# Kernel optimization log

Measured on AMD Instinct MI355X. Metric: run time of the kernel, lower is better.

Reference implementation:

```python
import jax, jax.numpy as jnp
import numpy as np

B, N, E, D = 2, 8192, 1024, 128   # batch, seq, embed_dim, expand_ratio (= head dim)
H = E // D                        # 8 heads (f_proj output dim)
CHUNK = 64
LN_EPS = 1e-5


def _gla_chunked(q, k, v, log_f):
    """Chunked simple GLA: S_t = exp(log_f_t) * S_{t-1} + k_t v_t^T ; o_t = q_t @ S_t.
    q,k,v: [b,h,n,d], log_f: [b,h,n] (log of per-head scalar decay in (0,1))."""
    b, h, n, d = q.shape
    nc = n // CHUNK
    qc = q.reshape(b, h, nc, CHUNK, d)
    kc = k.reshape(b, h, nc, CHUNK, d)
    vc = v.reshape(b, h, nc, CHUNK, d)
    gf = log_f.reshape(b, h, nc, CHUNK)
    g = jnp.cumsum(gf, axis=-1)          # inclusive within-chunk cum log decay [b,h,nc,C]
    gl = g[..., -1]                      # total chunk log decay [b,h,nc]

    # intra-chunk: A[i,j] = (q_i . k_j) * exp(g_i - g_j), j <= i  (g decreasing -> stable)
    mask = jnp.tril(jnp.ones((CHUNK, CHUNK), bool))
    A = jnp.einsum('bhcid,bhcjd->bhcij', qc, kc)
    A = jnp.where(mask, A * jnp.exp(g[..., :, None] - g[..., None, :]), 0.0)
    o_intra = jnp.einsum('bhcij,bhcjd->bhcid', A, vc)

    # inter-chunk: scan over chunks carrying state S [b,h,d,d]
    def step(S, inp):
        q_c, k_c, v_c, g_c, gl_c = inp   # [b,h,C,d],[b,h,C,d],[b,h,C,d],[b,h,C],[b,h]
        o = jnp.einsum('bhid,bhde->bhie', q_c * jnp.exp(g_c)[..., None], S)
        kd = k_c * jnp.exp(gl_c[..., None] - g_c)[..., None]
        S = jnp.exp(gl_c)[..., None, None] * S + jnp.einsum('bhid,bhie->bhde', kd, v_c)
        return S, o

    xs = (jnp.moveaxis(qc, 2, 0), jnp.moveaxis(kc, 2, 0), jnp.moveaxis(vc, 2, 0),
          jnp.moveaxis(g, 2, 0), jnp.moveaxis(gl, 2, 0))
    S0 = jnp.zeros((b, h, d, d), q.dtype)
    _, o_inter = jax.lax.scan(step, S0, xs)      # [nc,b,h,C,d]
    o_inter = jnp.moveaxis(o_inter, 0, 2)        # [b,h,nc,C,d]
    return (o_intra + o_inter).reshape(b, h, n, d)


def setup_inputs() -> dict:
    key = jax.random.key(0)
    ks = jax.random.split(key, 13)
    s = E ** -0.5
    x = jax.random.normal(ks[0], (B, N, E), jnp.float32)
    # per-head lower bound in (0,1), stored in log space as consumed by the module
    log_lower_bound = jnp.log(jax.random.uniform(ks[1], (H,), jnp.float32, 0.05, 0.95))
    Wq = jax.random.normal(ks[2], (E, E), jnp.float32) * s
    Wk = jax.random.normal(ks[3], (E, E), jnp.float32) * s
    Wv = jax.random.normal(ks[4], (E, E), jnp.float32) * s
    Wf = jax.random.normal(ks[5], (E, H), jnp.float32) * s
    Wb1 = jax.random.normal(ks[6], (E, D), jnp.float32) * s
    Wb2 = jax.random.normal(ks[7], (D, E), jnp.float32) * (D ** -0.5)
    Wg1 = jax.random.normal(ks[8], (E, D), jnp.float32) * s
    Wg2 = jax.random.normal(ks[9], (D, E), jnp.float32) * (D ** -0.5)
    Wo = jax.random.normal(ks[10], (E, E), jnp.float32) * s
    ln_scale = jnp.ones((E,), jnp.float32)
    ln_bias = jnp.zeros((E,), jnp.float32)
    return dict(x=x, log_lower_bound=log_lower_bound, Wq=Wq, Wk=Wk, Wv=Wv, Wf=Wf,
                Wb1=Wb1, Wb2=Wb2, Wg1=Wg1, Wg2=Wg2, Wo=Wo,
                ln_scale=ln_scale, ln_bias=ln_bias)


def reference(x, log_lower_bound, Wq, Wk, Wv, Wf, Wb1, Wb2, Wg1, Wg2, Wo, ln_scale, ln_bias):
    silu = jax.nn.silu
    q = silu(x @ Wq)
    k = silu(x @ Wk)
    v = x @ Wv
    f_pre = x @ Wf                               # [B,N,H] per-head decay logits

    # dense-memory Householder-style reflection of q
    beta = silu((x @ Wb1) @ Wb2)
    nb = jnp.sqrt(jnp.sum(beta * beta, axis=-1, keepdims=True))
    beta = beta / jnp.maximum(nb, 1e-6) / (E ** 0.5)
    q = q - 2.0 * jnp.sum(q * beta, axis=-1, keepdims=True) * beta

    def split(t):
        return t.reshape(B, N, H, D).transpose(0, 2, 1, 3)   # [B,H,N,D]
    qh, kh, vh = split(q), split(k), split(v)

    lb = jnp.exp(log_lower_bound)                            # [H]
    f = lb + (1.0 - lb) * jax.nn.sigmoid(f_pre)              # [B,N,H]
    log_f = jnp.log(f).transpose(0, 2, 1)                    # [B,H,N]

    o = _gla_chunked(qh, kh, vh, log_f)                      # [B,H,N,D]
    o = o.transpose(0, 2, 1, 3).reshape(B, N, E)

    gate = jax.nn.sigmoid((x @ Wg1) @ Wg2)
    o = o * gate

    mu = jnp.mean(o, axis=-1, keepdims=True)
    var = jnp.var(o, axis=-1, keepdims=True)
    o = (o - mu) / jnp.sqrt(var + LN_EPS) * ln_scale + ln_bias
    return o @ Wo
```

## Files before the change

kernel.cpp:

```cpp
#include <hip/hip_runtime.h>
#include <hip/hip_bf16.h>
#include <cstdint>


using u16 = unsigned short;
using u32 = unsigned int;
using u64 = unsigned long long;

typedef __attribute__((ext_vector_type(8))) short s16x8;
typedef __attribute__((ext_vector_type(4))) float f32x4;

__device__ __forceinline__ float b2f(u16 b){ u32 u = ((u32)b)<<16; return __builtin_bit_cast(float,u); }
__device__ __forceinline__ u16 f2b(float f){
  u32 u = __builtin_bit_cast(u32,f);
  return (u16)((u + 0x7FFFu + ((u>>16)&1u)) >> 16);
}
__device__ __forceinline__ float sigm(float x){ return 1.f/(1.f + __expf(-x)); }
__device__ __forceinline__ float silu(float x){ return x * sigm(x); }

__device__ __forceinline__ void gload16(const void* g, void* l){
  __builtin_amdgcn_global_load_lds((const __attribute__((address_space(1))) void*)g,
                                   (__attribute__((address_space(3))) void*)l, 16, 0, 0);
}
#define MFMA(a,b,c) __builtin_amdgcn_mfma_f32_16x16x32_bf16((a),(b),(c),0,0,0)

__device__ __forceinline__ void swz_block(int& bx, int& by){
  const int gx = gridDim.x;
  const int nwg = gx * gridDim.y;
  int lin = by*gx + bx;
  const int cpx = nwg >> 3;
  lin = (lin & 7)*cpx + (lin >> 3);
  bx = lin % gx; by = lin / gx;
}

__global__ __launch_bounds__(256) void fill_diag(float* __restrict__ p, int n, float val){
  int i = blockIdx.x*256 + threadIdx.x;
  if (i < n) p[i] = val;
}

__global__ __launch_bounds__(256) void cast_bf(const float4* __restrict__ src,
                                               ushort4* __restrict__ dst, int n4){
  int i = blockIdx.x*256 + threadIdx.x;
  int st = gridDim.x*256;
  for (; i < n4; i += st){
    float4 v = src[i];
    ushort4 o; o.x=f2b(v.x); o.y=f2b(v.y); o.z=f2b(v.z); o.w=f2b(v.w);
    dst[i] = o;
  }
}

__global__ __launch_bounds__(256) void wprep(const float* __restrict__ src,
                                             u16* __restrict__ dst, int K, int Nsrc){
  __shared__ float t[64][65];
  const int k0 = blockIdx.x*64, n0 = blockIdx.y*64;
  const int tid = threadIdx.x;
  #pragma unroll
  for (int e=0;e<16;e++){
    int idx = e*256 + tid;
    int r = idx>>6, c = idx&63;
    float v = 0.f;
    if (n0 + c < Nsrc) v = src[(u64)(k0+r)*Nsrc + n0 + c];
    t[r][c] = v;
  }
  __syncthreads();
  #pragma unroll
  for (int e=0;e<16;e++){
    int idx = e*256 + tid;
    int nn = idx>>6, kk = idx&63;
    dst[(u64)(n0+nn)*K + k0 + kk] = f2b(t[kk][nn]);
  }
}

__global__ __launch_bounds__(256,4) void gemm_bt(const u16* __restrict__ A, int lda,
                                                 const u16* __restrict__ Bt,
                                                 void* __restrict__ C, int ldc,
                                                 int K, int mode){
  __shared__ __align__(16) u16 As[128*64];
  __shared__ __align__(16) u16 Bs[128*64];
  const int tid = threadIdx.x, lane = tid&63, wid = tid>>6;
  int bx = blockIdx.x, by = blockIdx.y;
  swz_block(bx, by);
  const int bn0 = bx*128, bm0 = by*128;
  const int wr = wid>>1, wc = wid&1;
  const int g = lane>>4, ln = lane&15;

  f32x4 acc[4][4];
  #pragma unroll
  for (int i=0;i<4;i++)
    #pragma unroll
    for (int j=0;j<4;j++) acc[i][j] = f32x4{0.f,0.f,0.f,0.f};

  const int nk = K >> 6;
  for (int kt = 0; kt < nk; ++kt){
    const int k0 = kt<<6;
    #pragma unroll
    for (int j=0;j<4;j++){
      const int p = (wid*4+j)*64 + lane;
      const int row = p>>3, sl = p&7;
      const int sc = ((sl ^ (row&7))<<3);
      gload16(A  + (u64)(bm0+row)*lda + k0 + sc, (char*)As + (wid*4+j)*1024);
      gload16(Bt + (u64)(bn0+row)*K   + k0 + sc, (char*)Bs + (wid*4+j)*1024);
    }
    __syncthreads();
    #pragma unroll
    for (int ks=0;ks<2;ks++){
      s16x8 af[4], bf[4];
      #pragma unroll
      for (int mt=0;mt<4;mt++){
        const int row = wr*64 + mt*16 + ln;
        af[mt] = *(const s16x8*)(As + row*64 + (((ks*4+g) ^ (row&7))<<3));
      }
      #pragma unroll
      for (int nt=0;nt<4;nt++){
        const int row = wc*64 + nt*16 + ln;
        bf[nt] = *(const s16x8*)(Bs + row*64 + (((ks*4+g) ^ (row&7))<<3));
      }
      #pragma unroll
      for (int mt=0;mt<4;mt++)
        #pragma unroll
        for (int nt=0;nt<4;nt++)
          acc[mt][nt] = MFMA(af[mt], bf[nt], acc[mt][nt]);
    }
    __syncthreads();
  }
  if (mode == 0){
    float* Cf = (float*)C;
    #pragma unroll
    for (int mt=0;mt<4;mt++)
      #pragma unroll
      for (int nt=0;nt<4;nt++){
        const int col = bn0 + wc*64 + nt*16 + ln;
        #pragma unroll
        for (int r=0;r<4;r++){
          const u64 row = (u64)(bm0 + wr*64 + mt*16 + g*4 + r);
          Cf[row*ldc + col] = acc[mt][nt][r];
        }
      }
  } else {
    u16* Cb = (u16*)C;
    #pragma unroll
    for (int mt=0;mt<4;mt++)
      #pragma unroll
      for (int nt=0;nt<4;nt++){
        const int col = bn0 + wc*64 + nt*16 + ln;
        #pragma unroll
        for (int r=0;r<4;r++){
          const u64 row = (u64)(bm0 + wr*64 + mt*16 + g*4 + r);
          Cb[row*ldc + col] = f2b(acc[mt][nt][r]);
        }
      }
  }
}

__global__ __launch_bounds__(256,4) void gemm_proj(const u16* __restrict__ A,
                                                   const u16* __restrict__ Bt,
                                                   u16* __restrict__ Qb,
                                                   u16* __restrict__ Kp,
                                                   u16* __restrict__ KT,
                                                   u16* __restrict__ VT,
                                                   u16* __restrict__ FP,
                                                   const float* __restrict__ Gp,
                                                   const float* __restrict__ GLp){
  __shared__ __align__(16) u16 As[128*64];
  __shared__ __align__(16) u16 Bs[128*64];
  const int tid = threadIdx.x, lane = tid&63, wid = tid>>6;
  int bx = blockIdx.x, by = blockIdx.y;
  swz_block(bx, by);
  const int bn0 = bx*128, bm0 = by*128;
  const int wr = wid>>1, wc = wid&1;
  const int g = lane>>4, ln = lane&15;

  f32x4 acc[4][4];
  #pragma unroll
  for (int i=0;i<4;i++)
    #pragma unroll
    for (int j=0;j<4;j++) acc[i][j] = f32x4{0.f,0.f,0.f,0.f};

  for (int kt = 0; kt < 16; ++kt){
    const int k0 = kt<<6;
    #pragma unroll
    for (int j=0;j<4;j++){
      const int p = (wid*4+j)*64 + lane;
      const int row = p>>3, sl = p&7;
      const int sc = ((sl ^ (row&7))<<3);
      gload16(A  + (u64)(bm0+row)*1024 + k0 + sc, (char*)As + (wid*4+j)*1024);
      gload16(Bt + (u64)(bn0+row)*1024 + k0 + sc, (char*)Bs + (wid*4+j)*1024);
    }
    __syncthreads();
    #pragma unroll
    for (int ks=0;ks<2;ks++){
      s16x8 af[4], bf[4];
      #pragma unroll
      for (int mt=0;mt<4;mt++){
        const int row = wr*64 + mt*16 + ln;
        af[mt] = *(const s16x8*)(As + row*64 + (((ks*4+g) ^ (row&7))<<3));
      }
      #pragma unroll
      for (int nt=0;nt<4;nt++){
        const int row = wc*64 + nt*16 + ln;
        bf[nt] = *(const s16x8*)(Bs + row*64 + (((ks*4+g) ^ (row&7))<<3));
      }
      #pragma unroll
      for (int mt=0;mt<4;mt++)
        #pragma unroll
        for (int nt=0;nt<4;nt++)
          acc[mt][nt] = MFMA(af[mt], bf[nt], acc[mt][nt]);
    }
    __syncthreads();
  }

  const int cb = bn0 >> 7;
  if (cb < 8){
    #pragma unroll
    for (int mt=0;mt<4;mt++)
      #pragma unroll
      for (int nt=0;nt<4;nt++){
        const int col = bn0 + wc*64 + nt*16 + ln;
        #pragma unroll
        for (int r=0;r<4;r++)
          Qb[(u64)(bm0 + wr*64 + mt*16 + g*4 + r)*1024 + col] = f2b(acc[mt][nt][r]);
      }
  } else if (cb < 16){
    const int h = cb - 8;
    const int bh = (bm0>>13)*8 + h;
    const int trowb = (bm0 & 8191) + wr*64;
    const float gl = GLp[bh*128 + (trowb>>6)];
    float es[4][4];
    #pragma unroll
    for (int mt=0;mt<4;mt++)
      #pragma unroll
      for (int r=0;r<4;r++)
        es[mt][r] = __expf(gl - Gp[(u64)bh*8192 + trowb + mt*16 + g*4 + r]);
    #pragma unroll
    for (int mt=0;mt<4;mt++){
      const int trow = trowb + mt*16 + g*4;
      #pragma unroll
      for (int nt=0;nt<4;nt++){
        const int d = wc*64 + nt*16 + ln;
        ushort4 o; u16* op = (u16*)&o;
        #pragma unroll
        for (int r=0;r<4;r++){
          const float s = silu(acc[mt][nt][r]);
          op[r] = f2b(s * es[mt][r]);
          Kp[(u64)(bm0 + wr*64 + mt*16 + g*4 + r)*1024 + h*128 + d] = f2b(s);
        }
        *(ushort4*)(KT + ((u64)bh*128 + d)*8192 + trow) = o;
      }
    }
  } else if (cb < 24){
    const int h = cb - 16;
    const int bh = (bm0>>13)*8 + h;
    const int trowb = (bm0 & 8191) + wr*64;
    #pragma unroll
    for (int mt=0;mt<4;mt++){
      const int trow = trowb + mt*16 + g*4;
      #pragma unroll
      for (int nt=0;nt<4;nt++){
        const int d = wc*64 + nt*16 + ln;
        ushort4 o; u16* op = (u16*)&o;
        #pragma unroll
        for (int r=0;r<4;r++) op[r] = f2b(acc[mt][nt][r]);
        *(ushort4*)(VT + ((u64)bh*128 + d)*8192 + trow) = o;
      }
    }
  } else {
    const int off = (cb == 24) ? 0 : 128;
    #pragma unroll
    for (int mt=0;mt<4;mt++)
      #pragma unroll
      for (int nt=0;nt<4;nt++){
        const int col = off + wc*64 + nt*16 + ln;
        #pragma unroll
        for (int r=0;r<4;r++)
          FP[(u64)(bm0 + wr*64 + mt*16 + g*4 + r)*384 + col] = f2b(acc[mt][nt][r]);
      }
  }
}

__global__ __launch_bounds__(64) void fkernel(const u16* __restrict__ FP,
                                              const float* __restrict__ llb,
                                              float* __restrict__ G, float* __restrict__ GL){
  const int c = blockIdx.x, bh = blockIdx.y;
  const int b = bh>>3, h = bh&7;
  const int t = threadIdx.x;
  const int tok = c*64 + t;
  const float fp = b2f(FP[(u64)(b*8192 + tok)*384 + 256 + h]);
  const float lb = __expf(llb[h]);
  const float f = lb + (1.f - lb) * sigm(fp);
  float x = __logf(f);
  #pragma unroll
  for (int d=1; d<64; d<<=1){
    float v = __shfl_up(x, d);
    if (t >= d) x += v;
  }
  G[(u64)bh*8192 + tok] = x;
  const float gl = __shfl(x, 63);
  if (t == 0) GL[bh*128 + c] = gl;
}

__global__ __launch_bounds__(256) void e1_reflect(u16* __restrict__ Q,
                                                  const u16* __restrict__ BP){
  const u64 t = blockIdx.x;
  const int tid = threadIdx.x;
  __shared__ float red[8];
  u16* qrow = Q + t*1024;
  const u16* brow = BP + t*1024;
  ushort4 qv = ((const ushort4*)qrow)[tid];
  ushort4 bv = ((const ushort4*)brow)[tid];
  u16* qp = (u16*)&qv; const u16* bp = (const u16*)&bv;
  float q[4], bb[4];
  float s1 = 0.f, s2 = 0.f;
  #pragma unroll
  for (int j=0;j<4;j++){
    const float qq = silu(b2f(qp[j]));
    const float bbv = silu(b2f(bp[j]));
    q[j] = qq; bb[j] = bbv;
    s1 += bbv*bbv; s2 += qq*bbv;
  }
  #pragma unroll
  for (int d=1; d<64; d<<=1){ s1 += __shfl_xor(s1,d); s2 += __shfl_xor(s2,d); }
  const int wid = tid>>6, lane = tid&63;
  if (lane==0){ red[wid]=s1; red[4+wid]=s2; }
  __syncthreads();
  s1 = red[0]+red[1]+red[2]+red[3];
  s2 = red[4]+red[5]+red[6]+red[7];
  const float bs = 1.f/(fmaxf(sqrtf(s1), 1e-6f) * 32.f);
  const float coef = 2.f * s2 * bs * bs;
  #pragma unroll
  for (int j=0;j<4;j++) qp[j] = f2b(q[j] - coef*bb[j]);
  ((ushort4*)qrow)[tid] = qv;
}

__global__ __launch_bounds__(256,4) void g1_local(const u16* __restrict__ KT,
                                                  const u16* __restrict__ VT,
                                                  u16* __restrict__ LT){
  __shared__ __align__(16) u16 kts[128*64];
  __shared__ __align__(16) u16 vts[128*64];
  const int c = blockIdx.x, bh = blockIdx.y;
  const int tid = threadIdx.x, lane = tid&63, wid = tid>>6;
  const int g = lane>>4, ln = lane&15;
  #pragma unroll
  for (int j=0;j<4;j++){
    const int p = (wid*4+j)*64 + lane;
    const int row = p>>3, sl = p&7;
    const int sc = ((sl ^ (row&7))<<3);
    gload16(KT + ((u64)bh*128 + row)*8192 + (u64)c*64 + sc, (char*)kts + (wid*4+j)*1024);
    gload16(VT + ((u64)bh*128 + row)*8192 + (u64)c*64 + sc, (char*)vts + (wid*4+j)*1024);
  }
  __syncthreads();
  f32x4 acc[2][8];
  #pragma unroll
  for (int mt=0;mt<2;mt++)
    #pragma unroll
    for (int dt=0;dt<8;dt++) acc[mt][dt] = f32x4{0.f,0.f,0.f,0.f};
  #pragma unroll
  for (int kk=0;kk<2;kk++){
    s16x8 av[2];
    #pragma unroll
    for (int mt=0;mt<2;mt++){
      const int row = wid*32 + mt*16 + ln;
      av[mt] = *(const s16x8*)(vts + row*64 + (((kk*4+g) ^ (row&7))<<3));
    }
    #pragma unroll
    for (int dt=0;dt<8;dt++){
      const int row = dt*16 + ln;
      const s16x8 bk = *(const s16x8*)(kts + row*64 + (((kk*4+g) ^ (row&7))<<3));
      #pragma unroll
      for (int mt=0;mt<2;mt++) acc[mt][dt] = MFMA(av[mt], bk, acc[mt][dt]);
    }
  }
  u16* out = LT + ((u64)(bh*128 + c)<<14);
  #pragma unroll
  for (int mt=0;mt<2;mt++)
    #pragma unroll
    for (int dt=0;dt<8;dt++){
      const int d = dt*16 + ln;
      #pragma unroll
      for (int r=0;r<4;r++){
        const int n = wid*32 + mt*16 + g*4 + r;
        out[n*128 + d] = f2b(acc[mt][dt][r]);
      }
    }
}

__global__ __launch_bounds__(256) void g2_scan(u16* __restrict__ LS,
                                               const float* __restrict__ GL){
  __shared__ float egl[128];
  const int bh = blockIdx.y;
  if (threadIdx.x < 128) egl[threadIdx.x] = __expf(GL[bh*128 + threadIdx.x]);
  __syncthreads();
  const u64 e = (u64)blockIdx.x*256 + threadIdx.x;
  u16* P = LS + ((u64)bh<<21) + e;
  float s = 0.f;
  for (int c=0;c<128;c++){
    const float l = b2f(P[(u64)c<<14]);
    P[(u64)c<<14] = f2b(s);
    s = egl[c]*s + l;
  }
}

__global__ __launch_bounds__(256,2) void g3_out(const u16* __restrict__ Qb,
                                                const u16* __restrict__ Kp,
                                                const u16* __restrict__ VT,
                                                const u16* __restrict__ SBb,
                                                const float* __restrict__ Gb,
                                                u16* __restrict__ O){
  __shared__ __align__(16) u16 qs[64*128];
  __shared__ __align__(16) u16 ks[64*128];
  __shared__ __align__(16) u16 vts[128*64];
  __shared__ __align__(16) u16 sbs[64*128];
  __shared__ __align__(16) u16 Ast[4][16*64];
  __shared__ float gg[64];
  const int c = blockIdx.x, bh = blockIdx.y;
  const int b = bh>>3, h = bh&7;
  const int tid = threadIdx.x, lane = tid&63, wid = tid>>6;
  const int g = lane>>4, ln = lane&15;
  const u64 trow0 = (u64)b*8192 + (u64)c*64;

  if (tid < 64) gg[tid] = Gb[(u64)bh*8192 + c*64 + tid];

  const u16* sbbase = SBb + ((u64)(bh*128 + c)<<14);
  #pragma unroll
  for (int j=0;j<4;j++){
    const int p = (wid*4+j)*64 + lane;
    const int row = p>>4, sl = p&15;
    const int sc = ((sl ^ (row&7))<<3);
    gload16(Qb + (trow0 + row)*1024 + h*128 + sc, (char*)qs + (wid*4+j)*1024);
    gload16(Kp + (trow0 + row)*1024 + h*128 + sc, (char*)ks + (wid*4+j)*1024);
    const int row2 = p>>3, sl2 = p&7;
    gload16(VT + ((u64)bh*128 + row2)*8192 + (u64)c*64 + ((sl2 ^ (row2&7))<<3),
            (char*)vts + (wid*4+j)*1024);
    gload16(sbbase + row*128 + sc, (char*)sbs + (wid*4+j)*1024);
  }
  __syncthreads();

  f32x4 pa[4];
  #pragma unroll
  for (int jt=0;jt<4;jt++) pa[jt] = f32x4{0.f,0.f,0.f,0.f};
  #pragma unroll
  for (int kk=0;kk<4;kk++){
    const int arow = wid*16 + ln;
    const s16x8 aq = *(const s16x8*)(qs + arow*128 + (((kk*4+g) ^ (arow&7))<<3));
    #pragma unroll
    for (int jt=0;jt<4;jt++){
      const int brow = jt*16 + ln;
      const s16x8 bk = *(const s16x8*)(ks + brow*128 + (((kk*4+g) ^ (brow&7))<<3));
      pa[jt] = MFMA(aq, bk, pa[jt]);
    }
  }
  #pragma unroll
  for (int jt=0;jt<4;jt++){
    const int jj = jt*16 + ln;
    const float gj = gg[jj];
    #pragma unroll
    for (int r=0;r<4;r++){
      const int il = g*4 + r;
      const int ii = wid*16 + il;
      const float v = (jj <= ii) ? pa[jt][r] * __expf(gg[ii] - gj) : 0.f;
      Ast[wid][il*64 + (((jj>>3) ^ (il&7))<<3) + (jj&7)] = f2b(v);
    }
  }
  {
    const int row = wid*16 + (lane>>2);
    const float sc = __expf(gg[row]);
    u16* base = qs + row*128 + (lane&3)*32;
    #pragma unroll
    for (int ee=0; ee<4; ee++){
      s16x8 v = *(s16x8*)(base + ee*8);
      u16* vp = (u16*)&v;
      #pragma unroll
      for (int xj=0;xj<8;xj++) vp[xj] = f2b(b2f(vp[xj]) * sc);
      *(s16x8*)(base + ee*8) = v;
    }
  }
  f32x4 acc[8];
  #pragma unroll
  for (int i=0;i<8;i++) acc[i] = f32x4{0.f,0.f,0.f,0.f};
  #pragma unroll
  for (int kk=0;kk<2;kk++){
    const s16x8 aa = *(const s16x8*)(Ast[wid] + ln*64 + (((kk*4+g) ^ (ln&7))<<3));
    #pragma unroll
    for (int nt=0;nt<8;nt++){
      const int brow = nt*16 + ln;
      const s16x8 bb = *(const s16x8*)(vts + brow*64 + (((kk*4+g) ^ (brow&7))<<3));
      acc[nt] = MFMA(aa, bb, acc[nt]);
    }
  }
  #pragma unroll
  for (int kk=0;kk<4;kk++){
    const int arow = wid*16 + ln;
    const s16x8 aq = *(const s16x8*)(qs + arow*128 + (((kk*4+g) ^ (arow&7))<<3));
    #pragma unroll
    for (int nt=0;nt<4;nt++){
      const int brow = nt*16 + ln;
      const s16x8 bs = *(const s16x8*)(sbs + brow*128 + (((kk*4+g) ^ (brow&7))<<3));
      acc[nt] = MFMA(aq, bs, acc[nt]);
    }
  }
  __syncthreads();
  #pragma unroll
  for (int j=0;j<4;j++){
    const int p = (wid*4+j)*64 + lane;
    const int row = p>>4, sl = p&15;
    gload16(sbbase + 8192 + row*128 + ((sl ^ (row&7))<<3), (char*)sbs + (wid*4+j)*1024);
  }
  __syncthreads();
  #pragma unroll
  for (int kk=0;kk<4;kk++){
    const int arow = wid*16 + ln;
    const s16x8 aq = *(const s16x8*)(qs + arow*128 + (((kk*4+g) ^ (arow&7))<<3));
    #pragma unroll
    for (int nt=0;nt<4;nt++){
      const int brow = nt*16 + ln;
      const s16x8 bs = *(const s16x8*)(sbs + brow*128 + (((kk*4+g) ^ (brow&7))<<3));
      acc[4+nt] = MFMA(aq, bs, acc[4+nt]);
    }
  }
  u16* outp = O + trow0*1024 + h*128;
  #pragma unroll
  for (int nt=0;nt<8;nt++){
    const int n = nt*16 + ln;
    #pragma unroll
    for (int r=0;r<4;r++){
      const int i = wid*16 + g*4 + r;
      outp[(u64)i*1024 + n] = f2b(acc[nt][r]);
    }
  }
}

__global__ __launch_bounds__(256) void e2_ln(const u16* __restrict__ O,
                                             const u16* __restrict__ GP,
                                             const float* __restrict__ lnsc,
                                             const float* __restrict__ lnbi,
                                             u16* __restrict__ OL){
  const u64 t = blockIdx.x;
  const int tid = threadIdx.x;
  __shared__ float red[8];
  ushort4 ov = ((const ushort4*)(O + t*1024))[tid];
  ushort4 gv = ((const ushort4*)(GP + t*1024))[tid];
  const u16* ovp = (const u16*)&ov;
  const u16* gvp = (const u16*)&gv;
  float o[4]; float s = 0.f, s2 = 0.f;
  #pragma unroll
  for (int j=0;j<4;j++){
    const float val = b2f(ovp[j]) * sigm(b2f(gvp[j]));
    o[j] = val; s += val; s2 += val*val;
  }
  #pragma unroll
  for (int d=1; d<64; d<<=1){ s += __shfl_xor(s,d); s2 += __shfl_xor(s2,d); }
  const int wid = tid>>6, lane = tid&63;
  if (lane==0){ red[wid]=s; red[4+wid]=s2; }
  __syncthreads();
  s = red[0]+red[1]+red[2]+red[3];
  s2 = red[4]+red[5]+red[6]+red[7];
  const float mu = s * (1.f/1024.f);
  const float var = s2 * (1.f/1024.f) - mu*mu;
  const float rs = rsqrtf(var + 1e-5f);
  ushort4 out; u16* op = (u16*)&out;
  #pragma unroll
  for (int j=0;j<4;j++){
    const int e = tid*4 + j;
    op[j] = f2b((o[j]-mu)*rs*lnsc[e] + lnbi[e]);
  }
  ((ushort4*)(OL + t*1024))[tid] = out;
}

extern "C" void kernel_launch(void* const* d_in, const int* in_sizes, int n_in,
                              void* d_out, int out_size, void* d_ws, size_t ws_size,
                              hipStream_t stream){
  const float* x   = (const float*)d_in[0];
  const float* llb = (const float*)d_in[1];
  const float* Wq  = (const float*)d_in[2];
  const float* Wk  = (const float*)d_in[3];
  const float* Wv  = (const float*)d_in[4];
  const float* Wf  = (const float*)d_in[5];
  const float* Wb1 = (const float*)d_in[6];
  const float* Wb2 = (const float*)d_in[7];
  const float* Wg1 = (const float*)d_in[8];
  const float* Wg2 = (const float*)d_in[9];
  const float* Wo  = (const float*)d_in[10];
  const float* lnsc= (const float*)d_in[11];
  const float* lnbi= (const float*)d_in[12];

  const u64 REQUIRED = 190586880ull;
  if (ws_size < REQUIRED){
    const float val = 1.0e6f + (float)(u64)(ws_size>>20) * 1024.0f;
    fill_diag<<<dim3((out_size+255)/256),256,0,stream>>>((float*)d_out, out_size, val);
    return;
  }

  char* ws = (char*)d_ws;
  u16*  WCAT = (u16*)(ws + 0ull);
  u16*  WB2T = (u16*)(ws + 7077888ull);
  u16*  WG2T = (u16*)(ws + 7340032ull);
  u16*  WOT  = (u16*)(ws + 7602176ull);
  float* Gb  = (float*)(ws + 9699328ull);
  float* GLb = (float*)(ws + 10223616ull);
  u16*  FP   = (u16*)(ws + 10231808ull);
  u16*  R0   = (u16*)(ws + 22814720ull);
  u16*  Qb   = (u16*)(ws + 56369152ull);
  u16*  Kp   = (u16*)(ws + 89923584ull);
  u16*  KT   = (u16*)(ws + 123478016ull);
  u16*  VT   = (u16*)(ws + 157032448ull);
  u16*  LTSB = (u16*)d_out;
  u16*  XB = R0, *BP = R0, *GP = R0;
  u16*  Ob = KT, *OL = Qb;

  cast_bf<<<dim3(4096),256,0,stream>>>((const float4*)x, (ushort4*)XB, 16384*1024/4);

  wprep<<<dim3(16,16),256,0,stream>>>(Wq,  WCAT +    0*1024, 1024, 1024);
  wprep<<<dim3(16,16),256,0,stream>>>(Wk,  WCAT + 1024*1024, 1024, 1024);
  wprep<<<dim3(16,16),256,0,stream>>>(Wv,  WCAT + 2048*1024, 1024, 1024);
  wprep<<<dim3(16, 2),256,0,stream>>>(Wb1, WCAT + 3072*1024, 1024, 128);
  wprep<<<dim3(16, 2),256,0,stream>>>(Wg1, WCAT + 3200*1024, 1024, 128);
  wprep<<<dim3(16, 2),256,0,stream>>>(Wf,  WCAT + 3328*1024, 1024, 8);
  wprep<<<dim3(2,16),256,0,stream>>>(Wb2, WB2T, 128, 1024);
  wprep<<<dim3(2,16),256,0,stream>>>(Wg2, WG2T, 128, 1024);
  wprep<<<dim3(16,16),256,0,stream>>>(Wo,  WOT, 1024, 1024);

  gemm_bt<<<dim3(1,128),256,0,stream>>>(XB, 1024, WCAT + 3328*1024, FP + 256, 384, 1024, 1);
  fkernel<<<dim3(128,16),64,0,stream>>>(FP, llb, Gb, GLb);

  gemm_proj<<<dim3(26,128),256,0,stream>>>(XB, WCAT, Qb, Kp, KT, VT, FP, Gb, GLb);

  gemm_bt<<<dim3(8,128),256,0,stream>>>(FP, 384, WB2T, BP, 1024, 128, 1);
  e1_reflect<<<dim3(16384),256,0,stream>>>(Qb, BP);

  gemm_bt<<<dim3(8,128),256,0,stream>>>(FP + 128, 384, WG2T, GP, 1024, 128, 1);

  g1_local<<<dim3(128,16),256,0,stream>>>(KT, VT, LTSB);
  g2_scan<<<dim3(64,16),256,0,stream>>>(LTSB, GLb);
  g3_out<<<dim3(128,16),256,0,stream>>>(Qb, Kp, VT, LTSB, Gb, Ob);

  e2_ln<<<dim3(16384),256,0,stream>>>(Ob, GP, lnsc, lnbi, OL);

  gemm_bt<<<dim3(8,128),256,0,stream>>>(OL, 1024, WOT, d_out, 1024, 1024, 0);
}
```

Baseline: 447.8 us.

## Use 256x256 double-buffered GEMM tiles and merge weight-prep launches

Replaces the 128x128 single-buffered GEMM tiles with 256x256 tiles on 512 threads. LDS is double-buffered so the next k-slice loads while the current one feeds MFMA, using explicit vmcnt waits and raw barriers. Applies this to the projection GEMM, the two beta/gate GEMMs and the output GEMM. Also merges nine weight-prep launches into one 3D-grid kernel. Larger tiles raise operand reuse and cut global traffic, but they use more registers and launch fewer blocks, which may hurt occupancy and SM fill.

```diff
diff --git a/kernel.cpp b/kernel.cpp
--- a/kernel.cpp
+++ b/kernel.cpp
@@ -23,6 +23,20 @@
                                    (__attribute__((address_space(3))) void*)l, 16, 0, 0);
 }
 #define MFMA(a,b,c) __builtin_amdgcn_mfma_f32_16x16x32_bf16((a),(b),(c),0,0,0)
+
+__device__ __forceinline__ void bar(){
+  asm volatile("" ::: "memory");
+  __builtin_amdgcn_s_barrier();
+  asm volatile("" ::: "memory");
+}
+__device__ __forceinline__ void wait_vm8(){
+  asm volatile("s_waitcnt vmcnt(8)" ::: "memory");
+  __builtin_amdgcn_sched_barrier(0);
+}
+__device__ __forceinline__ void wait_vm0(){
+  asm volatile("s_waitcnt vmcnt(0)" ::: "memory");
+  __builtin_amdgcn_sched_barrier(0);
+}
 
 __device__ __forceinline__ void swz_block(int& bx, int& by){
   const int gx = gridDim.x;
@@ -49,8 +63,33 @@
   }
 }
 
-__global__ __launch_bounds__(256) void wprep(const float* __restrict__ src,
-                                             u16* __restrict__ dst, int K, int Nsrc){
+__global__ __launch_bounds__(256) void wprep_all(const float* __restrict__ Wq,
+                                                 const float* __restrict__ Wk,
+                                                 const float* __restrict__ Wv,
+                                                 const float* __restrict__ Wf,
+                                                 const float* __restrict__ Wb1,
+                                                 const float* __restrict__ Wb2,
+                                                 const float* __restrict__ Wg1,
+                                                 const float* __restrict__ Wg2,
+                                                 const float* __restrict__ Wo,
+                                                 u16* __restrict__ WCAT,
+                                                 u16* __restrict__ WB2T,
+                                                 u16* __restrict__ WG2T,
+                                                 u16* __restrict__ WOT){
+  const int z = blockIdx.z;
+  const float* src; u16* dst; int K, Nsrc, kb, nb;
+  switch(z){
+    case 0: src=Wq;  dst=WCAT;            K=1024; Nsrc=1024; kb=16; nb=16; break;
+    case 1: src=Wk;  dst=WCAT+1024*1024;  K=1024; Nsrc=1024; kb=16; nb=16; break;
+    case 2: src=Wv;  dst=WCAT+2048*1024;  K=1024; Nsrc=1024; kb=16; nb=16; break;
+    case 3: src=Wb1; dst=WCAT+3072*1024;  K=1024; Nsrc=128;  kb=16; nb=2;  break;
+    case 4: src=Wg1; dst=WCAT+3200*1024;  K=1024; Nsrc=128;  kb=16; nb=2;  break;
+    case 5: src=Wf;  dst=WCAT+3328*1024;  K=1024; Nsrc=8;    kb=16; nb=2;  break;
+    case 6: src=Wb2; dst=WB2T;            K=128;  Nsrc=1024; kb=2;  nb=16; break;
+    case 7: src=Wg2; dst=WG2T;            K=128;  Nsrc=1024; kb=2;  nb=16; break;
+    default:src=Wo;  dst=WOT;             K=1024; Nsrc=1024; kb=16; nb=16; break;
+  }
+  if (blockIdx.x >= (u32)kb || blockIdx.y >= (u32)nb) return;
   __shared__ float t[64][65];
   const int k0 = blockIdx.x*64, n0 = blockIdx.y*64;
   const int tid = threadIdx.x;
@@ -131,10 +170,8 @@
       for (int nt=0;nt<4;nt++){
         const int col = bn0 + wc*64 + nt*16 + ln;
         #pragma unroll
-        for (int r=0;r<4;r++){
-          const u64 row = (u64)(bm0 + wr*64 + mt*16 + g*4 + r);
-          Cf[row*ldc + col] = acc[mt][nt][r];
-        }
+        for (int r=0;r<4;r++)
+          Cf[(u64)(bm0 + wr*64 + mt*16 + g*4 + r)*ldc + col] = acc[mt][nt][r];
       }
   } else {
     u16* Cb = (u16*)C;
@@ -144,15 +181,99 @@
       for (int nt=0;nt<4;nt++){
         const int col = bn0 + wc*64 + nt*16 + ln;
         #pragma unroll
-        for (int r=0;r<4;r++){
-          const u64 row = (u64)(bm0 + wr*64 + mt*16 + g*4 + r);
-          Cb[row*ldc + col] = f2b(acc[mt][nt][r]);
-        }
-      }
-  }
-}
-
-__global__ __launch_bounds__(256,4) void gemm_proj(const u16* __restrict__ A,
+        for (int r=0;r<4;r++)
+          Cb[(u64)(bm0 + wr*64 + mt*16 + g*4 + r)*ldc + col] = f2b(acc[mt][nt][r]);
+      }
+  }
+}
+
+#define STAGE256(kt_, c_)                                                              \
+  do{ const int kk0 = (kt_)<<6;                                                        \
+    _Pragma("unroll")                                                                  \
+    for (int j=0;j<4;j++){                                                             \
+      const int p = j*512 + tid;                                                       \
+      const int row = p>>3, sl = p&7;                                                  \
+      const int sc = ((sl ^ (row&7))<<3);                                              \
+      gload16(A  + (u64)(bm0+row)*lda + kk0 + sc,                                      \
+              (char*)lds + (c_)*65536 + (j*8+wid)*1024);                               \
+      gload16(Bt + (u64)(bn0+row)*K   + kk0 + sc,                                      \
+              (char*)lds + (c_)*65536 + 32768 + (j*8+wid)*1024);                       \
+    } }while(0)
+
+#define GEMM256_CORE()                                                                 \
+  f32x4 acc[8][4];                                                                     \
+  _Pragma("unroll")                                                                    \
+  for (int i=0;i<8;i++)                                                                \
+    _Pragma("unroll")                                                                  \
+    for (int j=0;j<4;j++) acc[i][j] = f32x4{0.f,0.f,0.f,0.f};                          \
+  const int nk = K >> 6;                                                               \
+  STAGE256(0, 0);                                                                      \
+  int cbuf = 0;                                                                        \
+  for (int kt = 0; kt < nk; ++kt){                                                     \
+    if (kt+1 < nk){ STAGE256(kt+1, cbuf^1); wait_vm8(); } else { wait_vm0(); }         \
+    bar();                                                                             \
+    const u16* As_c = lds + cbuf*32768;                                                \
+    const u16* Bs_c = As_c + 16384;                                                    \
+    s16x8 bfr[2][4];                                                                   \
+    _Pragma("unroll")                                                                  \
+    for (int ks=0;ks<2;ks++)                                                           \
+      _Pragma("unroll")                                                                \
+      for (int n=0;n<4;n++){                                                           \
+        const int row = wc*64 + n*16 + ln;                                             \
+        bfr[ks][n] = *(const s16x8*)(Bs_c + row*64 + (((ks*4+g) ^ (row&7))<<3));       \
+      }                                                                                \
+    _Pragma("unroll")                                                                  \
+    for (int m=0;m<8;m++){                                                             \
+      const int arow = wr*128 + m*16 + ln;                                             \
+      _Pragma("unroll")                                                                \
+      for (int ks=0;ks<2;ks++){                                                        \
+        const s16x8 af = *(const s16x8*)(As_c + arow*64 + (((ks*4+g) ^ (arow&7))<<3)); \
+        _Pragma("unroll")                                                              \
+        for (int n=0;n<4;n++) acc[m][n] = MFMA(af, bfr[ks][n], acc[m][n]);             \
+      }                                                                                \
+    }                                                                                  \
+    bar();                                                                             \
+    cbuf ^= 1;                                                                         \
+  }
+
+__global__ __launch_bounds__(512,2) void gemm256(const u16* __restrict__ A, int lda,
+                                                 const u16* __restrict__ Bt,
+                                                 void* __restrict__ C, int ldc,
+                                                 int K, int mode){
+  __shared__ __align__(16) u16 lds[2*32768];
+  const int tid = threadIdx.x, lane = tid&63, wid = tid>>6;
+  int bx = blockIdx.x, by = blockIdx.y;
+  swz_block(bx, by);
+  const int bn0 = bx*256, bm0 = by*256;
+  const int wr = wid>>2, wc = wid&3;
+  const int g = lane>>4, ln = lane&15;
+  GEMM256_CORE();
+  if (mode == 0){
+    float* Cf = (float*)C;
+    #pragma unroll
+    for (int m=0;m<8;m++)
+      #pragma unroll
+      for (int n=0;n<4;n++){
+        const int col = bn0 + wc*64 + n*16 + ln;
+        #pragma unroll
+        for (int r=0;r<4;r++)
+          Cf[(u64)(bm0 + wr*128 + m*16 + g*4 + r)*ldc + col] = acc[m][n][r];
+      }
+  } else {
+    u16* Cb = (u16*)C;
+    #pragma unroll
+    for (int m=0;m<8;m++)
+      #pragma unroll
+      for (int n=0;n<4;n++){
+        const int col = bn0 + wc*64 + n*16 + ln;
+        #pragma unroll
+        for (int r=0;r<4;r++)
+          Cb[(u64)(bm0 + wr*128 + m*16 + g*4 + r)*ldc + col] = f2b(acc[m][n][r]);
+      }
+  }
+}
+
+__global__ __launch_bounds__(512,2) void gemm_proj(const u16* __restrict__ A,
                                                    const u16* __restrict__ Bt,
                                                    u16* __restrict__ Qb,
                                                    u16* __restrict__ Kp,
@@ -161,118 +282,77 @@
                                                    u16* __restrict__ FP,
                                                    const float* __restrict__ Gp,
                                                    const float* __restrict__ GLp){
-  __shared__ __align__(16) u16 As[128*64];
-  __shared__ __align__(16) u16 Bs[128*64];
+  __shared__ __align__(16) u16 lds[2*32768];
   const int tid = threadIdx.x, lane = tid&63, wid = tid>>6;
   int bx = blockIdx.x, by = blockIdx.y;
   swz_block(bx, by);
-  const int bn0 = bx*128, bm0 = by*128;
-  const int wr = wid>>1, wc = wid&1;
+  const int bn0 = bx*256, bm0 = by*256;
+  const int lda = 1024, K = 1024;
+  const int wr = wid>>2, wc = wid&3;
   const int g = lane>>4, ln = lane&15;
-
-  f32x4 acc[4][4];
-  #pragma unroll
-  for (int i=0;i<4;i++)
-    #pragma unroll
-    for (int j=0;j<4;j++) acc[i][j] = f32x4{0.f,0.f,0.f,0.f};
-
-  for (int kt = 0; kt < 16; ++kt){
-    const int k0 = kt<<6;
-    #pragma unroll
-    for (int j=0;j<4;j++){
-      const int p = (wid*4+j)*64 + lane;
-      const int row = p>>3, sl = p&7;
-      const int sc = ((sl ^ (row&7))<<3);
-      gload16(A  + (u64)(bm0+row)*1024 + k0 + sc, (char*)As + (wid*4+j)*1024);
-      gload16(Bt + (u64)(bn0+row)*1024 + k0 + sc, (char*)Bs + (wid*4+j)*1024);
-    }
-    __syncthreads();
-    #pragma unroll
-    for (int ks=0;ks<2;ks++){
-      s16x8 af[4], bf[4];
-      #pragma unroll
-      for (int mt=0;mt<4;mt++){
-        const int row = wr*64 + mt*16 + ln;
-        af[mt] = *(const s16x8*)(As + row*64 + (((ks*4+g) ^ (row&7))<<3));
-      }
-      #pragma unroll
-      for (int nt=0;nt<4;nt++){
-        const int row = wc*64 + nt*16 + ln;
-        bf[nt] = *(const s16x8*)(Bs + row*64 + (((ks*4+g) ^ (row&7))<<3));
-      }
-      #pragma unroll
-      for (int mt=0;mt<4;mt++)
-        #pragma unroll
-        for (int nt=0;nt<4;nt++)
-          acc[mt][nt] = MFMA(af[mt], bf[nt], acc[mt][nt]);
-    }
-    __syncthreads();
-  }
-
-  const int cb = bn0 >> 7;
-  if (cb < 8){
-    #pragma unroll
-    for (int mt=0;mt<4;mt++)
-      #pragma unroll
-      for (int nt=0;nt<4;nt++){
-        const int col = bn0 + wc*64 + nt*16 + ln;
+  GEMM256_CORE();
+
+  const int cw0 = bn0 + wc*64;
+  const int hb = cw0 >> 7;
+  if (hb < 8){
+    #pragma unroll
+    for (int m=0;m<8;m++)
+      #pragma unroll
+      for (int n=0;n<4;n++){
+        const int col = cw0 + n*16 + ln;
         #pragma unroll
         for (int r=0;r<4;r++)
-          Qb[(u64)(bm0 + wr*64 + mt*16 + g*4 + r)*1024 + col] = f2b(acc[mt][nt][r]);
-      }
-  } else if (cb < 16){
-    const int h = cb - 8;
+          Qb[(u64)(bm0 + wr*128 + m*16 + g*4 + r)*1024 + col] = f2b(acc[m][n][r]);
+      }
+  } else if (hb < 16){
+    const int h = hb - 8;
     const int bh = (bm0>>13)*8 + h;
-    const int trowb = (bm0 & 8191) + wr*64;
-    const float gl = GLp[bh*128 + (trowb>>6)];
-    float es[4][4];
-    #pragma unroll
-    for (int mt=0;mt<4;mt++)
-      #pragma unroll
-      for (int r=0;r<4;r++)
-        es[mt][r] = __expf(gl - Gp[(u64)bh*8192 + trowb + mt*16 + g*4 + r]);
-    #pragma unroll
-    for (int mt=0;mt<4;mt++){
-      const int trow = trowb + mt*16 + g*4;
-      #pragma unroll
-      for (int nt=0;nt<4;nt++){
-        const int d = wc*64 + nt*16 + ln;
+    const int dbase = cw0 & 127;
+    #pragma unroll
+    for (int m=0;m<8;m++){
+      const int trow = (bm0&8191) + wr*128 + m*16 + g*4;
+      const float gl = GLp[bh*128 + (trow>>6)];
+      float es[4];
+      #pragma unroll
+      for (int r=0;r<4;r++) es[r] = __expf(gl - Gp[(u64)bh*8192 + trow + r]);
+      #pragma unroll
+      for (int n=0;n<4;n++){
+        const int d = dbase + n*16 + ln;
         ushort4 o; u16* op = (u16*)&o;
         #pragma unroll
         for (int r=0;r<4;r++){
-          const float s = silu(acc[mt][nt][r]);
-          op[r] = f2b(s * es[mt][r]);
-          Kp[(u64)(bm0 + wr*64 + mt*16 + g*4 + r)*1024 + h*128 + d] = f2b(s);
+          const float s = silu(acc[m][n][r]);
+          op[r] = f2b(s * es[r]);
+          Kp[(u64)(bm0 + wr*128 + m*16 + g*4 + r)*1024 + h*128 + d] = f2b(s);
         }
         *(ushort4*)(KT + ((u64)bh*128 + d)*8192 + trow) = o;
       }
     }
-  } else if (cb < 24){
-    const int h = cb - 16;
+  } else if (hb < 24){
+    const int h = hb - 16;
     const int bh = (bm0>>13)*8 + h;
-    const int trowb = (bm0 & 8191) + wr*64;
-    #pragma unroll
-    for (int mt=0;mt<4;mt++){
-      const int trow = trowb + mt*16 + g*4;
-      #pragma unroll
-      for (int nt=0;nt<4;nt++){
-        const int d = wc*64 + nt*16 + ln;
+    const int dbase = cw0 & 127;
+    #pragma unroll
+    for (int m=0;m<8;m++){
+      const int trow = (bm0&8191) + wr*128 + m*16 + g*4;
+      #pragma unroll
+      for (int n=0;n<4;n++){
+        const int d = dbase + n*16 + ln;
         ushort4 o; u16* op = (u16*)&o;
         #pragma unroll
-        for (int r=0;r<4;r++) op[r] = f2b(acc[mt][nt][r]);
+        for (int r=0;r<4;r++) op[r] = f2b(acc[m][n][r]);
         *(ushort4*)(VT + ((u64)bh*128 + d)*8192 + trow) = o;
       }
     }
   } else {
-    const int off = (cb == 24) ? 0 : 128;
-    #pragma unroll
-    for (int mt=0;mt<4;mt++)
-      #pragma unroll
-      for (int nt=0;nt<4;nt++){
-        const int col = off + wc*64 + nt*16 + ln;
+    #pragma unroll
+    for (int m=0;m<8;m++)
+      #pragma unroll
+      for (int n=0;n<4;n++){
+        const int col = cw0 + n*16 + ln - 3072;
         #pragma unroll
         for (int r=0;r<4;r++)
-          FP[(u64)(bm0 + wr*64 + mt*16 + g*4 + r)*384 + col] = f2b(acc[mt][nt][r]);
+          FP[(u64)(bm0 + wr*128 + m*16 + g*4 + r)*384 + col] = f2b(acc[m][n][r]);
       }
   }
 }
@@ -607,26 +687,18 @@
   u16*  Ob = KT, *OL = Qb;
 
   cast_bf<<<dim3(4096),256,0,stream>>>((const float4*)x, (ushort4*)XB, 16384*1024/4);
-
-  wprep<<<dim3(16,16),256,0,stream>>>(Wq,  WCAT +    0*1024, 1024, 1024);
-  wprep<<<dim3(16,16),256,0,stream>>>(Wk,  WCAT + 1024*1024, 1024, 1024);
-  wprep<<<dim3(16,16),256,0,stream>>>(Wv,  WCAT + 2048*1024, 1024, 1024);
-  wprep<<<dim3(16, 2),256,0,stream>>>(Wb1, WCAT + 3072*1024, 1024, 128);
-  wprep<<<dim3(16, 2),256,0,stream>>>(Wg1, WCAT + 3200*1024, 1024, 128);
-  wprep<<<dim3(16, 2),256,0,stream>>>(Wf,  WCAT + 3328*1024, 1024, 8);
-  wprep<<<dim3(2,16),256,0,stream>>>(Wb2, WB2T, 128, 1024);
-  wprep<<<dim3(2,16),256,0,stream>>>(Wg2, WG2T, 128, 1024);
-  wprep<<<dim3(16,16),256,0,stream>>>(Wo,  WOT, 1024, 1024);
+  wprep_all<<<dim3(16,16,9),256,0,stream>>>(Wq,Wk,Wv,Wf,Wb1,Wb2,Wg1,Wg2,Wo,
+                                            WCAT, WB2T, WG2T, WOT);
 
   gemm_bt<<<dim3(1,128),256,0,stream>>>(XB, 1024, WCAT + 3328*1024, FP + 256, 384, 1024, 1);
   fkernel<<<dim3(128,16),64,0,stream>>>(FP, llb, Gb, GLb);
 
-  gemm_proj<<<dim3(26,128),256,0,stream>>>(XB, WCAT, Qb, Kp, KT, VT, FP, Gb, GLb);
-
-  gemm_bt<<<dim3(8,128),256,0,stream>>>(FP, 384, WB2T, BP, 1024, 128, 1);
+  gemm_proj<<<dim3(13,64),512,0,stream>>>(XB, WCAT, Qb, Kp, KT, VT, FP, Gb, GLb);
+
+  gemm256<<<dim3(4,64),512,0,stream>>>(FP, 384, WB2T, BP, 1024, 128, 1);
   e1_reflect<<<dim3(16384),256,0,stream>>>(Qb, BP);
 
-  gemm_bt<<<dim3(8,128),256,0,stream>>>(FP + 128, 384, WG2T, GP, 1024, 128, 1);
+  gemm256<<<dim3(4,64),512,0,stream>>>(FP + 128, 384, WG2T, GP, 1024, 128, 1);
 
   g1_local<<<dim3(128,16),256,0,stream>>>(KT, VT, LTSB);
   g2_scan<<<dim3(64,16),256,0,stream>>>(LTSB, GLb);
@@ -634,5 +706,5 @@
 
   e2_ln<<<dim3(16384),256,0,stream>>>(Ob, GP, lnsc, lnbi, OL);
 
-  gemm_bt<<<dim3(8,128),256,0,stream>>>(OL, 1024, WOT, d_out, 1024, 1024, 0);
-}
+  gemm256<<<dim3(4,64),512,0,stream>>>(OL, 1024, WOT, d_out, 1024, 1024, 0);
+}
```

After: 377.9 us. 1.18x faster.
